# Optimization experiments

Hardware: AMD Instinct MI355X
Metric: run time of the kernel (lower is better)

Reference implementation:

```python
import jax, jax.numpy as jnp
import numpy as np
from jax import lax

T, B, C = 2048, 8, 1024
H, K, P = 16, 31, 15  # num_heads, kernel_size, padding_l
R = C // H


def setup_inputs() -> dict:
    key = jax.random.key(0)
    k1, k2 = jax.random.split(key)
    x = jax.random.normal(k1, (T, B, C), dtype=jnp.float32)
    # xavier_uniform for (H, 1, K): gain*sqrt(6/(fan_in+fan_out)) with fan_in=K, fan_out=1
    limit = float(np.sqrt(6.0 / (K + 1)))
    weight = jax.random.uniform(k2, (H, 1, K), dtype=jnp.float32, minval=-limit, maxval=limit)
    bias = jnp.zeros((C,), dtype=jnp.float32)
    return {"x": x, "weight": weight, "bias": bias}


def reference(x, weight, bias):
    # x: (T, B, C); weight: (H, 1, K); bias: (C,)
    w = jax.nn.softmax(weight.reshape(H, K), axis=1)       # weight_softmax=True
    w_ch = jnp.repeat(w, R, axis=0)                        # (C, K) per-channel depthwise filters
    x_nct = jnp.transpose(x, (1, 2, 0))                    # (B, C, T)
    # depthwise cross-correlation, 'same' padding: left P, right K-1-P
    out = lax.conv_general_dilated(
        x_nct, w_ch[:, None, :],                           # kernel (O=C, I/g=1, K)
        window_strides=(1,), padding=[(P, K - 1 - P)],
        feature_group_count=C,
        dimension_numbers=("NCH", "OIH", "NCH"),
    )                                                      # (B, C, T)
    return jnp.transpose(out, (2, 0, 1)) + bias            # (T, B, C)
```

## Files before the change

kernel.cpp:

```cpp
#include <hip/hip_runtime.h>
#include <math.h>


#define T_DIM 2048
#define B_DIM 8
#define C_DIM 1024
#define H_DIM 16
#define K_DIM 31
#define P_PAD 15

#define T_TILE 128
#define C_TILE 64
#define NWAVE 4
#define STRIP (T_TILE / NWAVE)
#define ROWS (T_TILE + K_DIM - 1)

__global__ __launch_bounds__(256, 4) void lwconv_tbc_kernel(
    const float* __restrict__ x,
    const float* __restrict__ weight,
    const float* __restrict__ bias,
    float* __restrict__ out)
{
    __shared__ float s_x[ROWS * C_TILE];
    __shared__ float s_w[K_DIM];

    const int cTile = blockIdx.x;
    const int b     = blockIdx.y;
    const int tTile = blockIdx.z;
    const int c0 = cTile * C_TILE;
    const int h  = cTile;
    const int t0 = tTile * T_TILE;
    const int tid = threadIdx.x;

    if (tid == 0) {
        float wv[K_DIM];
        float m = -1e30f;
        for (int k = 0; k < K_DIM; ++k) {
            wv[k] = weight[h * K_DIM + k];
            m = fmaxf(m, wv[k]);
        }
        float s = 0.f;
        for (int k = 0; k < K_DIM; ++k) { wv[k] = expf(wv[k] - m); s += wv[k]; }
        const float inv = 1.f / s;
        for (int k = 0; k < K_DIM; ++k) s_w[k] = wv[k] * inv;
    }

    const int NV4 = ROWS * (C_TILE / 4);
    for (int idx = tid; idx < NV4; idx += 256) {
        const int row = idx >> 4;
        const int c4  = idx & 15;
        const int t   = t0 - P_PAD + row;
        float4 v = make_float4(0.f, 0.f, 0.f, 0.f);
        if (t >= 0 && t < T_DIM) {
            v = *reinterpret_cast<const float4*>(
                    &x[((size_t)t * B_DIM + b) * C_DIM + c0 + c4 * 4]);
        }
        *reinterpret_cast<float4*>(&s_x[row * C_TILE + c4 * 4]) = v;
    }
    __syncthreads();

    float w[K_DIM];
    #pragma unroll
    for (int k = 0; k < K_DIM; ++k) w[k] = s_w[k];

    const int lane  = tid & 63;
    const int strip = tid >> 6;
    const int c = c0 + lane;
    const float bv = bias[c];

    const int r0 = strip * STRIP;
    float win[K_DIM];
    #pragma unroll
    for (int k = 0; k < K_DIM; ++k) win[k] = s_x[(r0 + k) * C_TILE + lane];

    #pragma unroll
    for (int i = 0; i < STRIP; ++i) {
        float acc = bv;
        #pragma unroll
        for (int k = 0; k < K_DIM; ++k) acc = fmaf(win[k], w[k], acc);
        const int t = t0 + r0 + i;
        out[((size_t)t * B_DIM + b) * C_DIM + c] = acc;
        if (i < STRIP - 1) {
            #pragma unroll
            for (int k = 0; k < K_DIM - 1; ++k) win[k] = win[k + 1];
            win[K_DIM - 1] = s_x[(r0 + i + K_DIM) * C_TILE + lane];
        }
    }
}

extern "C" void kernel_launch(void* const* d_in, const int* in_sizes, int n_in,
                              void* d_out, int out_size, void* d_ws, size_t ws_size,
                              hipStream_t stream) {
    const float* x      = (const float*)d_in[0];
    const float* weight = (const float*)d_in[1];
    const float* bias   = (const float*)d_in[2];
    float* out = (float*)d_out;

    dim3 grid(C_DIM / C_TILE, B_DIM, T_DIM / T_TILE);
    dim3 block(256);
    lwconv_tbc_kernel<<<grid, block, 0, stream>>>(x, weight, bias, out);
}
```

Baseline: 32.88 us.

## Narrow channel tile, scatter-accumulate outputs per loaded row, scalarize weights

Halves the channel tile to 32 so each block spans 32 channels and 8 time strips of 16 rows, doubling the block count and raising the occupancy hint to 8 blocks. The sliding-window loop is replaced by an output-stationary form: each shared-memory row is loaded once and FMA'd into 16 register accumulators, which removes the register-shift copies. Weights are forced into scalar registers via readfirstlane. The 32-wide channel tile means each wave covers two time strips and global writes are 128-byte segments, which may reduce coalescing efficiency.

```diff
diff --git a/kernel.cpp b/kernel.cpp
--- a/kernel.cpp
+++ b/kernel.cpp
@@ -10,12 +10,11 @@
 #define P_PAD 15
 
 #define T_TILE 128
-#define C_TILE 64
-#define NWAVE 4
-#define STRIP (T_TILE / NWAVE)
+#define C_TILE 32
 #define ROWS (T_TILE + K_DIM - 1)
+#define STRIP 16
 
-__global__ __launch_bounds__(256, 4) void lwconv_tbc_kernel(
+__global__ __launch_bounds__(256, 8) void lwconv_tbc_kernel(
     const float* __restrict__ x,
     const float* __restrict__ weight,
     const float* __restrict__ bias,
@@ -28,7 +27,7 @@
     const int b     = blockIdx.y;
     const int tTile = blockIdx.z;
     const int c0 = cTile * C_TILE;
-    const int h  = cTile;
+    const int h  = c0 >> 6;
     const int t0 = tTile * T_TILE;
     const int tid = threadIdx.x;
 
@@ -47,8 +46,8 @@
 
     const int NV4 = ROWS * (C_TILE / 4);
     for (int idx = tid; idx < NV4; idx += 256) {
-        const int row = idx >> 4;
-        const int c4  = idx & 15;
+        const int row = idx >> 3;
+        const int c4  = idx & 7;
         const int t   = t0 - P_PAD + row;
         float4 v = make_float4(0.f, 0.f, 0.f, 0.f);
         if (t >= 0 && t < T_DIM) {
@@ -61,30 +60,38 @@
 
     float w[K_DIM];
     #pragma unroll
-    for (int k = 0; k < K_DIM; ++k) w[k] = s_w[k];
+    for (int k = 0; k < K_DIM; ++k) {
+        union { float f; int i; } u;
+        u.f = s_w[k];
+        u.i = __builtin_amdgcn_readfirstlane(u.i);
+        w[k] = u.f;
+    }
 
-    const int lane  = tid & 63;
-    const int strip = tid >> 6;
-    const int c = c0 + lane;
+    const int ch    = tid & 31;
+    const int strip = tid >> 5;
+    const int c = c0 + ch;
     const float bv = bias[c];
+    const int r0 = strip * STRIP;
 
-    const int r0 = strip * STRIP;
-    float win[K_DIM];
+    float acc[STRIP];
     #pragma unroll
-    for (int k = 0; k < K_DIM; ++k) win[k] = s_x[(r0 + k) * C_TILE + lane];
+    for (int i = 0; i < STRIP; ++i) acc[i] = bv;
+
+    #pragma unroll
+    for (int r = 0; r < STRIP + K_DIM - 1; ++r) {
+        const float xv = s_x[(r0 + r) * C_TILE + ch];
+        #pragma unroll
+        for (int i = 0; i < STRIP; ++i) {
+            if (r - i >= 0 && r - i < K_DIM) {
+                acc[i] = fmaf(xv, w[r - i], acc[i]);
+            }
+        }
+    }
 
     #pragma unroll
     for (int i = 0; i < STRIP; ++i) {
-        float acc = bv;
-        #pragma unroll
-        for (int k = 0; k < K_DIM; ++k) acc = fmaf(win[k], w[k], acc);
         const int t = t0 + r0 + i;
-        out[((size_t)t * B_DIM + b) * C_DIM + c] = acc;
-        if (i < STRIP - 1) {
-            #pragma unroll
-            for (int k = 0; k < K_DIM - 1; ++k) win[k] = win[k + 1];
-            win[K_DIM - 1] = s_x[(r0 + i + K_DIM) * C_TILE + lane];
-        }
+        out[((size_t)t * B_DIM + b) * C_DIM + c] = acc[i];
     }
 }
 
```

After: 37.09 us. 12.8% more time.
